# Kernel optimization log

Hardware: AMD Instinct MI355X
Metric: run time of the kernel (lower is better)

Reference implementation:

```python
import jax, jax.numpy as jnp
import numpy as np
import math

B, S, E, H = 2, 4096, 1024, 1024

def setup_inputs() -> dict:
    key = jax.random.key(0)
    ks = jax.random.split(key, 7)
    X = jax.random.normal(ks[0], (B, S, E), dtype=jnp.float32)
    attention_mask = jnp.ones((B, S, S), dtype=jnp.int32)
    sc = 1.0 / math.sqrt(E)
    Wq = jax.random.normal(ks[1], (H, E), dtype=jnp.float32) * sc
    Wk = jax.random.normal(ks[2], (H, E), dtype=jnp.float32) * sc
    Wv = jax.random.normal(ks[3], (H, E), dtype=jnp.float32) * sc
    bq = jnp.zeros((H,), dtype=jnp.float32)
    bk = jnp.zeros((H,), dtype=jnp.float32)
    bv = jnp.zeros((H,), dtype=jnp.float32)
    return {"X": X, "attention_mask": attention_mask,
            "Wq": Wq, "bq": bq, "Wk": Wk, "bk": bk, "Wv": Wv, "bv": bv}

def reference(X, attention_mask, Wq, bq, Wk, bk, Wv, bv):
    # Linear layers: y = x @ W^T + b (torch convention W is [out, in])
    Q = jnp.einsum('bse,he->bsh', X, Wq) + bq
    K = jnp.einsum('bse,he->bsh', X, Wk) + bk
    V = jnp.einsum('bse,he->bsh', X, Wv) + bv
    scale = 1.0 / math.sqrt(H)
    scores = jnp.einsum('bqh,bkh->bqk', Q, K) * scale  # [B,S,S]
    scores = jnp.where(attention_mask == 0, -jnp.inf, scores)
    # dropout (eval mode -> identity) would be applied here, BEFORE softmax
    weights = jax.nn.softmax(scores, axis=-1)
    out = jnp.einsum('bqk,bkh->bqh', weights, V)  # [B,S,H]
    return out
```

## Files before the change

### kernel.cpp

```cpp
#include <hip/hip_runtime.h>
#include <stdint.h>


typedef __bf16 bf16;
typedef __attribute__((ext_vector_type(4))) __bf16 bf16x4;
typedef __attribute__((ext_vector_type(8))) __bf16 bf16x8;
typedef __attribute__((ext_vector_type(4))) float f32x4;

__device__ __forceinline__ void g2l16(const void* g, void* l) {
  __builtin_amdgcn_global_load_lds(
      (const __attribute__((address_space(1))) uint32_t*)g,
      (__attribute__((address_space(3))) uint32_t*)l, 16, 0, 0);
}

__device__ __forceinline__ f32x4 ds_read128(uint32_t addr) {
  f32x4 d;
  asm volatile("ds_read_b128 %0, %1" : "=v"(d) : "v"(addr));
  return d;
}

template <int V> struct IC { static constexpr int value = V; };
template <bool V> struct BC { static constexpr bool value = V; };

template <int N> __device__ __forceinline__ void waitvm() {
  if constexpr (N == 6) asm volatile("s_waitcnt vmcnt(6)" ::: "memory");
  else if constexpr (N == 4) asm volatile("s_waitcnt vmcnt(4)" ::: "memory");
  else if constexpr (N == 0) asm volatile("s_waitcnt vmcnt(0)" ::: "memory");
}

__global__ __launch_bounds__(256) void cvt_f32_bf16(
    const float* __restrict__ src, bf16* __restrict__ dst, int n) {
  const int i = (blockIdx.x * 256 + threadIdx.x) * 8;
  if (i >= n) return;
  f32x4 a = *(const f32x4*)(src + i);
  f32x4 b = *(const f32x4*)(src + i + 4);
  bf16x8 o;
#pragma unroll
  for (int e = 0; e < 4; ++e) { o[e] = (bf16)a[e]; o[4 + e] = (bf16)b[e]; }
  *(bf16x8*)(dst + i) = o;
}

__global__ __launch_bounds__(256) void cvt_w3(
    const float* __restrict__ Wq, const float* __restrict__ Wk,
    const float* __restrict__ Wv, bf16* __restrict__ dst) {
  const int i = (blockIdx.x * 256 + threadIdx.x) * 8;
  const int seg = i >> 20;
  const int off = i & 1048575;
  const float* src = (seg == 0) ? Wq : (seg == 1) ? Wk : Wv;
  f32x4 a = *(const f32x4*)(src + off);
  f32x4 b = *(const f32x4*)(src + off + 4);
  bf16x8 o;
#pragma unroll
  for (int e = 0; e < 4; ++e) { o[e] = (bf16)a[e]; o[4 + e] = (bf16)b[e]; }
  *(bf16x8*)(dst + i) = o;
}

__global__ __launch_bounds__(256) void pack_mask(
    const int* __restrict__ m, unsigned long long* __restrict__ bm,
    int n) {
  const int gw = (blockIdx.x * 256 + threadIdx.x) >> 6;
  const int lane = threadIdx.x & 63;
  const int nw = (2048 * 256) >> 6;
  for (int base = gw * 64; base < n; base += nw * 64) {
    const int v = m[base + lane];
    const unsigned long long b = __ballot(v != 0);
    if (lane == 0) bm[base >> 6] = b;
  }
}

template <int NT>
__device__ __forceinline__ void kloop256(
    const bf16* __restrict__ Ag, const bf16* __restrict__ Bg, const int KA,
    const int KB, bf16* lds, f32x4 (&acc)[8][4]) {
  const int tid = threadIdx.x;
  const int lane = tid & 63;
  const int wave = tid >> 6;
  const int l15 = lane & 15, quad = lane >> 4;
  const int wrow = (wave >> 2) * 128;
  const int wcol = (wave & 3) * 64;
  const int srow = tid >> 3;
  const int scol = ((tid & 7) ^ (srow & 7)) * 8;
  const int swz = l15 & 7;

  const uint32_t lds_u = (uint32_t)(uintptr_t)lds;
  const uint32_t a_l15 = lds_u + (uint32_t)((wrow + l15) * 128);
  const uint32_t b_l15 = lds_u + 32768u + (uint32_t)((wcol + l15) * 128);
  const uint32_t ck0 = (uint32_t)(((quad) ^ swz) * 16);
  const uint32_t ck1 = (uint32_t)(((4 + quad) ^ swz) * 16);

  auto stg = [&](int t, int h) {
    bf16* base = lds + (t & 1) * 32768;
    if (h == 0) {
      const bf16* g = Bg + (size_t)srow * KB + t * 64 + scol;
      g2l16(g, base + 16384 + tid * 8);
      g2l16(g + (size_t)64 * KB, base + 16384 + tid * 8 + 4096);
    } else if (h == 1) {
      const bf16* g = Bg + (size_t)(128 + srow) * KB + t * 64 + scol;
      g2l16(g, base + 24576 + tid * 8);
      g2l16(g + (size_t)64 * KB, base + 24576 + tid * 8 + 4096);
    } else if (h == 2) {
      const bf16* g = Ag + (size_t)srow * KA + t * 64 + scol;
      g2l16(g, base + tid * 8);
      g2l16(g + (size_t)128 * KA, base + tid * 8 + 8192);
    } else {
      const bf16* g = Ag + (size_t)(64 + srow) * KA + t * 64 + scol;
      g2l16(g, base + 4096 + tid * 8);
      g2l16(g + (size_t)128 * KA, base + 4096 + tid * 8 + 8192);
    }
  };

  f32x4 brf[2][4];
  auto phase = [&](int t, auto qc, int st, int sh, auto dsc, auto vmc) {
    constexpr int q = decltype(qc)::value;
    constexpr bool ds = decltype(dsc)::value;
    constexpr int vm = decltype(vmc)::value;
    const uint32_t bb = (t & 1) ? 65536u : 0u;
    f32x4 ar[2][2];
#pragma unroll
    for (int i = 0; i < 2; ++i) {
      ar[i][0] = ds_read128(a_l15 + bb + (uint32_t)((2 * q + i) * 2048) + ck0);
      ar[i][1] = ds_read128(a_l15 + bb + (uint32_t)((2 * q + i) * 2048) + ck1);
    }
    if constexpr (q == 0) {
#pragma unroll
      for (int j = 0; j < 4; ++j) {
        brf[0][j] = ds_read128(b_l15 + bb + (uint32_t)(j * 2048) + ck0);
        brf[1][j] = ds_read128(b_l15 + bb + (uint32_t)(j * 2048) + ck1);
      }
    }
    if constexpr (ds) stg(st, sh);
    __builtin_amdgcn_s_barrier();
    asm volatile("s_waitcnt lgkmcnt(0)" ::: "memory");
    __builtin_amdgcn_sched_barrier(0);
    __builtin_amdgcn_s_setprio(1);
#pragma unroll
    for (int ks = 0; ks < 2; ++ks)
#pragma unroll
      for (int i = 0; i < 2; ++i)
#pragma unroll
        for (int j = 0; j < 4; ++j)
          acc[2 * q + i][j] = __builtin_amdgcn_mfma_f32_16x16x32_bf16(
              __builtin_bit_cast(bf16x8, ar[i][ks]),
              __builtin_bit_cast(bf16x8, brf[ks][j]),
              acc[2 * q + i][j], 0, 0, 0);
    __builtin_amdgcn_s_setprio(0);
    waitvm<vm>();
    __builtin_amdgcn_s_barrier();
  };

  stg(0, 0); stg(0, 1); stg(0, 2); stg(0, 3);
  stg(1, 0); stg(1, 1); stg(1, 2);
  asm volatile("s_waitcnt vmcnt(6)" ::: "memory");
  __builtin_amdgcn_s_barrier();

  constexpr int NI = NT / 2;
#pragma unroll 1
  for (int u = 0; u < NI - 1; ++u) {
    const int t0 = 2 * u, t1 = t0 + 1;
    phase(t0, IC<0>{}, t1, 3, BC<true>{}, IC<-1>{});
    phase(t0, IC<1>{}, t0 + 2, 0, BC<true>{}, IC<-1>{});
    phase(t0, IC<2>{}, t0 + 2, 1, BC<true>{}, IC<-1>{});
    phase(t0, IC<3>{}, t0 + 2, 2, BC<true>{}, IC<6>{});
    phase(t1, IC<0>{}, t0 + 2, 3, BC<true>{}, IC<-1>{});
    phase(t1, IC<1>{}, t0 + 3, 0, BC<true>{}, IC<-1>{});
    phase(t1, IC<2>{}, t0 + 3, 1, BC<true>{}, IC<-1>{});
    phase(t1, IC<3>{}, t0 + 3, 2, BC<true>{}, IC<6>{});
  }
  {
    const int t0 = NT - 2, t1 = NT - 1;
    phase(t0, IC<0>{}, t1, 3, BC<true>{}, IC<-1>{});
    phase(t0, IC<1>{}, 0, 0, BC<false>{}, IC<-1>{});
    phase(t0, IC<2>{}, 0, 0, BC<false>{}, IC<-1>{});
    phase(t0, IC<3>{}, 0, 0, BC<false>{}, IC<0>{});
    phase(t1, IC<0>{}, 0, 0, BC<false>{}, IC<-1>{});
    phase(t1, IC<1>{}, 0, 0, BC<false>{}, IC<-1>{});
    phase(t1, IC<2>{}, 0, 0, BC<false>{}, IC<-1>{});
    phase(t1, IC<3>{}, 0, 0, BC<false>{}, IC<-1>{});
  }
}

__global__ __launch_bounds__(256, 2) void gemm_qkv(
    const bf16* __restrict__ Xb, const bf16* __restrict__ Wb3,
    const float* __restrict__ bq, const float* __restrict__ bk,
    const float* __restrict__ bv, bf16* __restrict__ QK,
    bf16* __restrict__ Vt)
{
  constexpr int K = 1024, N = 1024;
  __shared__ __align__(16) bf16 ldsA[128 * 64];
  __shared__ __align__(16) bf16 ldsB[128 * 64];

  const int tid  = threadIdx.x;
  const int lane = tid & 63;
  const int wave = tid >> 6;
  const int d = blockIdx.y * 64 + blockIdx.x;
  const int xcd = d & 7, slot = d >> 3;
  const int g = xcd * 8 + slot / 24;
  const int c = slot % 24;
  const int which = c >> 3;
  const int n0 = (c & 7) * 128;
  const int m0 = g * 128;
  const bf16* Bt = Wb3 + (size_t)which * 1048576;
  const float* bias = (which == 0) ? bq : ((which == 1) ? bk : bv);

  const int l15  = lane & 15;
  const int quad = lane >> 4;
  const int wm = (wave >> 1) * 64;
  const int wn = (wave & 1) * 64;
  const int sw = l15 & 7;

  f32x4 acc[4][4];
#pragma unroll
  for (int i = 0; i < 4; ++i)
#pragma unroll
    for (int j = 0; j < 4; ++j) acc[i][j] = f32x4{0.f, 0.f, 0.f, 0.f};

  const int srow = tid >> 3;
  const int scol = ((tid & 7) ^ (srow & 7)) * 8;
  const size_t a_base = (size_t)(m0 + srow) * K + scol;
  const size_t b_base = (size_t)(n0 + srow) * K + scol;
  const int lds_off = tid * 8;

  for (int kt = 0; kt < K; kt += 64) {
    const bf16* ga = Xb + a_base + kt;
    const bf16* gb = Bt + b_base + kt;
#pragma unroll
    for (int it = 0; it < 4; ++it) {
      g2l16(ga + (size_t)(it * 32) * K, &ldsA[lds_off + it * 2048]);
      g2l16(gb + (size_t)(it * 32) * K, &ldsB[lds_off + it * 2048]);
    }
    __syncthreads();
#pragma unroll
    for (int ks = 0; ks < 2; ++ks) {
      const int ch = ks * 4 + quad;
      bf16x8 af[4], bfg[4];
#pragma unroll
      for (int i = 0; i < 4; ++i)
        af[i] = *(const bf16x8*)&ldsA[(wm + i * 16 + l15) * 64 + (ch ^ sw) * 8];
#pragma unroll
      for (int j = 0; j < 4; ++j)
        bfg[j] = *(const bf16x8*)&ldsB[(wn + j * 16 + l15) * 64 + (ch ^ sw) * 8];
#pragma unroll
      for (int i = 0; i < 4; ++i)
#pragma unroll
        for (int j = 0; j < 4; ++j)
          acc[i][j] = __builtin_amdgcn_mfma_f32_16x16x32_bf16(
              af[i], bfg[j], acc[i][j], 0, 0, 0);
    }
    __syncthreads();
  }

  if (which < 2) {
    bf16* C = QK + (size_t)which * (size_t)(8192 * 1024);
#pragma unroll
    for (int i = 0; i < 4; ++i) {
#pragma unroll
      for (int j = 0; j < 4; ++j) {
        const int r = m0 + wm + i * 16 + quad * 4;
        const int cc = n0 + wn + j * 16 + l15;
        const float bvv = bias[cc];
        f32x4 v = acc[i][j];
#pragma unroll
        for (int reg = 0; reg < 4; ++reg)
          C[(size_t)(r + reg) * N + cc] = (bf16)(v[reg] + bvv);
      }
    }
  } else {
#pragma unroll
    for (int i = 0; i < 4; ++i) {
#pragma unroll
      for (int j = 0; j < 4; ++j) {
        const int r = m0 + wm + i * 16 + quad * 4;
        const int cc = n0 + wn + j * 16 + l15;
        const int b = r >> 12, s = r & 4095;
        const float bvv = bias[cc];
        f32x4 v = acc[i][j];
        bf16x4 o;
#pragma unroll
        for (int reg = 0; reg < 4; ++reg) o[reg] = (bf16)(v[reg] + bvv);
        *(bf16x4*)&Vt[((size_t)(b * 1024 + cc)) * 4096 + s] = o;
      }
    }
  }
}

__global__ __launch_bounds__(512, 2) void gemm_scores(
    const bf16* __restrict__ Q, const bf16* __restrict__ Kb,
    const unsigned long long* __restrict__ BM, bf16* __restrict__ P,
    float* __restrict__ row_sum) {
  __shared__ __align__(16) bf16 lds[2 * 32768];
  const int bid = blockIdx.y * 32 + blockIdx.x;
  const int sb = (bid & 7) * 64 + (bid >> 3);
  const int bx = sb & 31, by = sb >> 5;
  const int m0 = bx * 256;
  const int n0 = by * 256;
  const int batch = m0 >> 12;
  const bf16* Ag = Q + (size_t)m0 * 1024;
  const bf16* Bg = Kb + (size_t)batch * (size_t)(4096 * 1024) +
                   (size_t)n0 * 1024;

  f32x4 acc[8][4];
#pragma unroll
  for (int i = 0; i < 8; ++i)
#pragma unroll
    for (int j = 0; j < 4; ++j) acc[i][j] = f32x4{0.f, 0.f, 0.f, 0.f};

  kloop256<16>(Ag, Bg, 1024, 1024, lds, acc);

  const int lane = threadIdx.x & 63, wave = threadIdx.x >> 6;
  const int l15 = lane & 15, quad = lane >> 4;
  const int wrow = (wave >> 2) * 128, wcol = (wave & 3) * 64;
  const int bmcol = (n0 + wcol) >> 6;

#pragma unroll
  for (int i = 0; i < 8; ++i) {
    const int r = m0 + wrow + i * 16 + quad * 4;
    unsigned long long mrow[4];
#pragma unroll
    for (int reg = 0; reg < 4; ++reg)
      mrow[reg] = BM[(size_t)(r + reg) * 64 + bmcol];
    f32x4 rsum = f32x4{0.f, 0.f, 0.f, 0.f};
#pragma unroll
    for (int j = 0; j < 4; ++j) {
      const int c = n0 + wcol + j * 16 + l15;
      f32x4 v = acc[i][j];
#pragma unroll
      for (int reg = 0; reg < 4; ++reg) {
        float e = __expf(v[reg] * 0.03125f);
        if (((mrow[reg] >> (j * 16 + l15)) & 1ull) == 0) e = 0.f;
        P[(size_t)(r + reg) * 4096 + c] = (bf16)e;
        rsum[reg] += e;
      }
    }
#pragma unroll
    for (int off = 1; off < 16; off <<= 1) {
#pragma unroll
      for (int reg = 0; reg < 4; ++reg)
        rsum[reg] += __shfl_xor(rsum[reg], off);
    }
    if (l15 == 0) {
#pragma unroll
      for (int reg = 0; reg < 4; ++reg)
        atomicAdd(&row_sum[r + reg], rsum[reg]);
    }
  }
}

__global__ __launch_bounds__(256, 2) void gemm_pv(
    const bf16* __restrict__ A, const bf16* __restrict__ Bt,
    const float* __restrict__ row_sum, float* __restrict__ C)
{
  constexpr int N = 1024, K = 4096;
  __shared__ __align__(16) bf16 ldsA[128 * 64];
  __shared__ __align__(16) bf16 ldsB[128 * 64];

  const int tid  = threadIdx.x;
  const int lane = tid & 63;
  const int wave = tid >> 6;
  const int d = blockIdx.y * 64 + blockIdx.x;
  const int xcd = d & 7, slot = d >> 3;
  const int g = xcd * 8 + (slot >> 3);
  const int h = slot & 7;
  const int m0 = g * 128;
  const int n0 = h * 128;
  const int batch = m0 >> 12;
  const bf16* Btb = Bt + (size_t)batch * (size_t)(1024 * 4096);

  const int l15  = lane & 15;
  const int quad = lane >> 4;
  const int wm = (wave >> 1) * 64;
  const int wn = (wave & 1) * 64;
  const int sw = l15 & 7;

  f32x4 acc[4][4];
#pragma unroll
  for (int i = 0; i < 4; ++i)
#pragma unroll
    for (int j = 0; j < 4; ++j) acc[i][j] = f32x4{0.f, 0.f, 0.f, 0.f};

  const int srow = tid >> 3;
  const int scol = ((tid & 7) ^ (srow & 7)) * 8;
  const size_t a_base = (size_t)(m0 + srow) * K + scol;
  const size_t b_base = (size_t)(n0 + srow) * K + scol;
  const int lds_off = tid * 8;

  for (int kt = 0; kt < K; kt += 64) {
    const bf16* ga = A + a_base + kt;
    const bf16* gb = Btb + b_base + kt;
#pragma unroll
    for (int it = 0; it < 4; ++it) {
      g2l16(ga + (size_t)(it * 32) * K, &ldsA[lds_off + it * 2048]);
      g2l16(gb + (size_t)(it * 32) * K, &ldsB[lds_off + it * 2048]);
    }
    __syncthreads();
#pragma unroll
    for (int ks = 0; ks < 2; ++ks) {
      const int ch = ks * 4 + quad;
      bf16x8 af[4], bfg[4];
#pragma unroll
      for (int i = 0; i < 4; ++i)
        af[i] = *(const bf16x8*)&ldsA[(wm + i * 16 + l15) * 64 + (ch ^ sw) * 8];
#pragma unroll
      for (int j = 0; j < 4; ++j)
        bfg[j] = *(const bf16x8*)&ldsB[(wn + j * 16 + l15) * 64 + (ch ^ sw) * 8];
#pragma unroll
      for (int i = 0; i < 4; ++i)
#pragma unroll
        for (int j = 0; j < 4; ++j)
          acc[i][j] = __builtin_amdgcn_mfma_f32_16x16x32_bf16(
              af[i], bfg[j], acc[i][j], 0, 0, 0);
    }
    __syncthreads();
  }

#pragma unroll
  for (int i = 0; i < 4; ++i) {
    const int r = m0 + wm + i * 16 + quad * 4;
    f32x4 inv;
#pragma unroll
    for (int reg = 0; reg < 4; ++reg) inv[reg] = 1.0f / row_sum[r + reg];
#pragma unroll
    for (int j = 0; j < 4; ++j) {
      const int c = n0 + wn + j * 16 + l15;
      f32x4 v = acc[i][j];
#pragma unroll
      for (int reg = 0; reg < 4; ++reg)
        C[(size_t)(r + reg) * N + c] = v[reg] * inv[reg];
    }
  }
}

extern "C" void kernel_launch(void* const* d_in, const int* in_sizes, int n_in,
                              void* d_out, int out_size, void* d_ws,
                              size_t ws_size, hipStream_t stream) {
  const float* X   = (const float*)d_in[0];
  const int* mask  = (const int*)d_in[1];
  const float* Wq  = (const float*)d_in[2];
  const float* bq  = (const float*)d_in[3];
  const float* Wk  = (const float*)d_in[4];
  const float* bk  = (const float*)d_in[5];
  const float* Wv  = (const float*)d_in[6];
  const float* bv  = (const float*)d_in[7];
  float* out = (float*)d_out;

  const size_t QKV_ELEMS = (size_t)8192 * 1024;
  bf16* Q    = (bf16*)d_ws;
  bf16* Kb   = Q + QKV_ELEMS;
  bf16* X_bf = Kb + QKV_ELEMS;
  bf16* Vt   = X_bf + QKV_ELEMS;
  bf16* Sc   = Vt + QKV_ELEMS;
  bf16* W_bf = Sc;
  float* row_sum = (float*)X_bf;
  unsigned long long* BM =
      (unsigned long long*)((char*)X_bf + 65536);

  cvt_f32_bf16<<<dim3(4096), dim3(256), 0, stream>>>(X, X_bf, 8388608);
  cvt_w3<<<dim3(1536), dim3(256), 0, stream>>>(Wq, Wk, Wv, W_bf);
  gemm_qkv<<<dim3(64, 24), dim3(256), 0, stream>>>(X_bf, W_bf, bq, bk, bv, Q,
                                                   Vt);
  pack_mask<<<dim3(2048), dim3(256), 0, stream>>>(mask, BM, 33554432);
  hipMemsetAsync(row_sum, 0, 8192 * sizeof(float), stream);
  gemm_scores<<<dim3(32, 16), dim3(512), 0, stream>>>(Q, Kb, BM, Sc,
                                                      row_sum);
  gemm_pv<<<dim3(64, 8), dim3(256), 0, stream>>>(Sc, Vt, row_sum, out);
}
```

Measured before the change: 456.3 us.

## Fuse conversions, read mask directly in scores, replace atomics with partial sums

Merges the X and weight conversion kernels into a single launch. Removes the mask bit-packing kernel and the memset, so the scores epilogue reads the int32 mask directly. Row sums are now written as per-column-tile partials without atomics, and gemm_pv reduces 64 partials per row into LDS before normalizing. This trades fewer launches and no atomics for uncoalesced-ish int32 mask reads (128MB) inside the scores epilogue.

```diff
diff --git a/kernel.cpp b/kernel.cpp
--- a/kernel.cpp
+++ b/kernel.cpp
@@ -28,44 +28,37 @@
   else if constexpr (N == 0) asm volatile("s_waitcnt vmcnt(0)" ::: "memory");
 }
 
-__global__ __launch_bounds__(256) void cvt_f32_bf16(
-    const float* __restrict__ src, bf16* __restrict__ dst, int n) {
-  const int i = (blockIdx.x * 256 + threadIdx.x) * 8;
-  if (i >= n) return;
+__global__ __launch_bounds__(256) void cvt_all(
+    const float* __restrict__ X, const float* __restrict__ Wq,
+    const float* __restrict__ Wk, const float* __restrict__ Wv,
+    bf16* __restrict__ X_bf, bf16* __restrict__ W_bf) {
+  const int bid = blockIdx.x;
+  const float* src;
+  bf16* dst;
+  int i;
+  if (bid < 4096) {
+    i = (bid * 256 + threadIdx.x) * 8;
+    src = X; dst = X_bf;
+  } else {
+    i = ((bid - 4096) * 256 + threadIdx.x) * 8;
+    const int seg = i >> 20;
+    const int off = i & 1048575;
+    src = (seg == 0) ? Wq : (seg == 1) ? Wk : Wv;
+    dst = W_bf;
+    f32x4 a = *(const f32x4*)(src + off);
+    f32x4 b = *(const f32x4*)(src + off + 4);
+    bf16x8 o;
+#pragma unroll
+    for (int e = 0; e < 4; ++e) { o[e] = (bf16)a[e]; o[4 + e] = (bf16)b[e]; }
+    *(bf16x8*)(dst + i) = o;
+    return;
+  }
   f32x4 a = *(const f32x4*)(src + i);
   f32x4 b = *(const f32x4*)(src + i + 4);
   bf16x8 o;
 #pragma unroll
   for (int e = 0; e < 4; ++e) { o[e] = (bf16)a[e]; o[4 + e] = (bf16)b[e]; }
   *(bf16x8*)(dst + i) = o;
-}
-
-__global__ __launch_bounds__(256) void cvt_w3(
-    const float* __restrict__ Wq, const float* __restrict__ Wk,
-    const float* __restrict__ Wv, bf16* __restrict__ dst) {
-  const int i = (blockIdx.x * 256 + threadIdx.x) * 8;
-  const int seg = i >> 20;
-  const int off = i & 1048575;
-  const float* src = (seg == 0) ? Wq : (seg == 1) ? Wk : Wv;
-  f32x4 a = *(const f32x4*)(src + off);
-  f32x4 b = *(const f32x4*)(src + off + 4);
-  bf16x8 o;
-#pragma unroll
-  for (int e = 0; e < 4; ++e) { o[e] = (bf16)a[e]; o[4 + e] = (bf16)b[e]; }
-  *(bf16x8*)(dst + i) = o;
-}
-
-__global__ __launch_bounds__(256) void pack_mask(
-    const int* __restrict__ m, unsigned long long* __restrict__ bm,
-    int n) {
-  const int gw = (blockIdx.x * 256 + threadIdx.x) >> 6;
-  const int lane = threadIdx.x & 63;
-  const int nw = (2048 * 256) >> 6;
-  for (int base = gw * 64; base < n; base += nw * 64) {
-    const int v = m[base + lane];
-    const unsigned long long b = __ballot(v != 0);
-    if (lane == 0) bm[base >> 6] = b;
-  }
 }
 
 template <int NT>
@@ -285,8 +278,8 @@
 
 __global__ __launch_bounds__(512, 2) void gemm_scores(
     const bf16* __restrict__ Q, const bf16* __restrict__ Kb,
-    const unsigned long long* __restrict__ BM, bf16* __restrict__ P,
-    float* __restrict__ row_sum) {
+    const int* __restrict__ mask, bf16* __restrict__ P,
+    float* __restrict__ psum) {
   __shared__ __align__(16) bf16 lds[2 * 32768];
   const int bid = blockIdx.y * 32 + blockIdx.x;
   const int sb = (bid & 7) * 64 + (bid >> 3);
@@ -309,15 +302,11 @@
   const int lane = threadIdx.x & 63, wave = threadIdx.x >> 6;
   const int l15 = lane & 15, quad = lane >> 4;
   const int wrow = (wave >> 2) * 128, wcol = (wave & 3) * 64;
-  const int bmcol = (n0 + wcol) >> 6;
+  float* ps = psum + (size_t)(by * 4 + (wave & 3)) * 8192;
 
 #pragma unroll
   for (int i = 0; i < 8; ++i) {
     const int r = m0 + wrow + i * 16 + quad * 4;
-    unsigned long long mrow[4];
-#pragma unroll
-    for (int reg = 0; reg < 4; ++reg)
-      mrow[reg] = BM[(size_t)(r + reg) * 64 + bmcol];
     f32x4 rsum = f32x4{0.f, 0.f, 0.f, 0.f};
 #pragma unroll
     for (int j = 0; j < 4; ++j) {
@@ -326,7 +315,7 @@
 #pragma unroll
       for (int reg = 0; reg < 4; ++reg) {
         float e = __expf(v[reg] * 0.03125f);
-        if (((mrow[reg] >> (j * 16 + l15)) & 1ull) == 0) e = 0.f;
+        if (mask[(size_t)(r + reg) * 4096 + c] == 0) e = 0.f;
         P[(size_t)(r + reg) * 4096 + c] = (bf16)e;
         rsum[reg] += e;
       }
@@ -339,15 +328,14 @@
     }
     if (l15 == 0) {
 #pragma unroll
-      for (int reg = 0; reg < 4; ++reg)
-        atomicAdd(&row_sum[r + reg], rsum[reg]);
+      for (int reg = 0; reg < 4; ++reg) ps[r + reg] = rsum[reg];
     }
   }
 }
 
 __global__ __launch_bounds__(256, 2) void gemm_pv(
     const bf16* __restrict__ A, const bf16* __restrict__ Bt,
-    const float* __restrict__ row_sum, float* __restrict__ C)
+    const float* __restrict__ psum, float* __restrict__ C)
 {
   constexpr int N = 1024, K = 4096;
   __shared__ __align__(16) bf16 ldsA[128 * 64];
@@ -412,12 +400,22 @@
     __syncthreads();
   }
 
+  float* linv = (float*)ldsA;
+  if (tid < 128) {
+    float s = 0.f;
+#pragma unroll 8
+    for (int p = 0; p < 64; ++p) s += psum[(size_t)p * 8192 + m0 + tid];
+    linv[tid] = 1.0f / s;
+  }
+  __syncthreads();
+
 #pragma unroll
   for (int i = 0; i < 4; ++i) {
-    const int r = m0 + wm + i * 16 + quad * 4;
+    const int lr = wm + i * 16 + quad * 4;
+    const int r = m0 + lr;
     f32x4 inv;
 #pragma unroll
-    for (int reg = 0; reg < 4; ++reg) inv[reg] = 1.0f / row_sum[r + reg];
+    for (int reg = 0; reg < 4; ++reg) inv[reg] = linv[lr + reg];
 #pragma unroll
     for (int j = 0; j < 4; ++j) {
       const int c = n0 + wn + j * 16 + l15;
@@ -449,17 +447,11 @@
   bf16* Vt   = X_bf + QKV_ELEMS;
   bf16* Sc   = Vt + QKV_ELEMS;
   bf16* W_bf = Sc;
-  float* row_sum = (float*)X_bf;
-  unsigned long long* BM =
-      (unsigned long long*)((char*)X_bf + 65536);
-
-  cvt_f32_bf16<<<dim3(4096), dim3(256), 0, stream>>>(X, X_bf, 8388608);
-  cvt_w3<<<dim3(1536), dim3(256), 0, stream>>>(Wq, Wk, Wv, W_bf);
+  float* psum = (float*)X_bf;
+
+  cvt_all<<<dim3(5632), dim3(256), 0, stream>>>(X, Wq, Wk, Wv, X_bf, W_bf);
   gemm_qkv<<<dim3(64, 24), dim3(256), 0, stream>>>(X_bf, W_bf, bq, bk, bv, Q,
                                                    Vt);
-  pack_mask<<<dim3(2048), dim3(256), 0, stream>>>(mask, BM, 33554432);
-  hipMemsetAsync(row_sum, 0, 8192 * sizeof(float), stream);
-  gemm_scores<<<dim3(32, 16), dim3(512), 0, stream>>>(Q, Kb, BM, Sc,
-                                                      row_sum);
-  gemm_pv<<<dim3(64, 8), dim3(256), 0, stream>>>(Sc, Vt, row_sum, out);
-}
+  gemm_scores<<<dim3(32, 16), dim3(512), 0, stream>>>(Q, Kb, mask, Sc, psum);
+  gemm_pv<<<dim3(64, 8), dim3(256), 0, stream>>>(Sc, Vt, psum, out);
+}
```

Result: faster. 414.6 us (-9.1%).
